# Performance work log

Hardware: AMD Instinct MI355X
Metric: run time of the kernel (lower is better)

The kernel has to match this reference:

```python
import jax, jax.numpy as jnp
import numpy as np

B, T, C, H, N = 2, 1024, 2048, 32, 64
KVH = 8                       # GQA kv heads
KV = KVH * N                  # 512
REP = H // KVH                # 4
EPS = 1e-6
LORA = [96, 96, 64, 256, 64]  # xw, xa, xv, xg, xk lora dims


def rmsnorm(x, w, eps=EPS):
    xf = x.astype(jnp.float32)
    var = jnp.mean(xf * xf, axis=-1, keepdims=True)
    return (w * (xf * jax.lax.rsqrt(var + eps))).astype(x.dtype)


def rotate_half(x):
    x1, x2 = jnp.split(x, 2, axis=-1)
    return jnp.concatenate([-x2, x1], axis=-1)


def rwkv7_scan(r, w, k, v, a, b, state0):
    # r,w,k,v,a,b: [B,T,H,N]; state0: [B,H,N,N] (value x key)
    # per step: S = S*exp(w) + (S@a) b^T + v k^T ; o = S @ r
    def step(S, inp):
        r_t, w_t, k_t, v_t, a_t, b_t = inp  # each [B,H,N]
        sa = jnp.einsum('bhvk,bhk->bhv', S, a_t)
        S = (S * jnp.exp(w_t)[:, :, None, :]
             + sa[..., None] * b_t[:, :, None, :]
             + v_t[..., None] * k_t[:, :, None, :])
        o = jnp.einsum('bhvk,bhk->bhv', S, r_t)
        return S, o
    seqs = tuple(jnp.moveaxis(t, 1, 0) for t in (r, w, k, v, a, b))
    S, o = jax.lax.scan(step, state0, seqs)
    return jnp.moveaxis(o, 0, 1), S


def setup_inputs() -> dict:
    key = jax.random.key(0)
    ks = jax.random.split(key, 24)
    g = lambda i, shape, s=0.02: jax.random.normal(ks[i], shape, jnp.float32) * s
    # real rope cache, theta = 1e6, rotary_dim = N
    pos = jnp.arange(T, dtype=jnp.float32)
    inv = 1.0 / (1e6 ** (jnp.arange(0, N, 2, dtype=jnp.float32) / N))
    ang = pos[:, None] * inv[None, :]
    ang = jnp.concatenate([ang, ang], axis=-1)  # [T, N]
    cos = jnp.broadcast_to(jnp.cos(ang)[None], (B, T, N))
    sin = jnp.broadcast_to(jnp.sin(ang)[None], (B, T, N))
    return dict(
        x_in=jax.random.normal(ks[0], (B, T, C), jnp.float32),
        v_first=jax.random.normal(ks[1], (B, T, KVH, N), jnp.float32),
        k_first=jax.random.normal(ks[2], (B, T, KVH, N), jnp.float32),
        state=jnp.zeros((B, H, N, N), jnp.float32),
        calc_cos=cos, calc_sin=sin,
        ln1=jnp.ones((C,), jnp.float32), ln2=jnp.ones((C,), jnp.float32),
        ln_r=jnp.ones((N,), jnp.float32), ln_k=jnp.ones((N,), jnp.float32),
        wavgk1=g(3, (C, sum(LORA))),
        w0=g(4, (H * N,)), w2=g(5, (LORA[0], H * N)),
        a0=g(6, (H * N,)), a2=g(7, (LORA[1], H * N)),
        v0=g(8, (KV,)), v2=g(9, (LORA[2], KV)),
        k0=g(10, (KV,)), k2=g(11, (LORA[4], KV)),
        g2=g(12, (LORA[3], H * N)),
        r_k=g(13, (H, N)),
        RKV_W=g(14, (C, H * N + 2 * KV)),
        O_W=g(15, (H * N, C)),
        R_bias=g(16, (H * N,)), K_bias=g(17, (KV,)), V_bias=g(18, (KV,)),
    )


def _forward(x_in, v_first, k_first, state, calc_cos, calc_sin,
             ln1, ln2, ln_r, ln_k, wavgk1, w0, w2, a0, a2, v0, v2,
             k0, k2, g2, r_k, RKV_W, O_W, R_bias, K_bias, V_bias):
    x = rmsnorm(x_in, ln1)
    xw, xa, xv, xg, xk = jnp.split(x @ wavgk1, np.cumsum(LORA)[:-1].tolist(), axis=-1)
    r, k, v = jnp.split(x @ RKV_W, [H * N, H * N + KV], axis=-1)
    r = (r + R_bias).reshape(B, T, H, N)
    k = (k + K_bias).reshape(B, T, KVH, N)
    v = (v + V_bias).reshape(B, T, KVH, N)
    r = rmsnorm(r, ln_r)
    k = rmsnorm(k, ln_k)
    cos = calc_cos[:, :, None, :]
    sin = calc_sin[:, :, None, :]
    r = r * cos + rotate_half(r) * sin
    k = k * cos + rotate_half(k) * sin
    # layer_id != 0: sigmoid-gated interpolation toward first-layer v/k
    v = v + (v_first - v) * jax.nn.sigmoid(xv @ v2 + v0).reshape(B, T, KVH, N)
    k = k + (k_first - k) * jax.nn.sigmoid(xk @ k2 + k0).reshape(B, T, KVH, N)
    # GQA repeat (contiguous per kv head, as repeat_kv does)
    k = jnp.repeat(k, REP, axis=2).reshape(B, T, H * N)
    v = jnp.repeat(v, REP, axis=2).reshape(B, T, H * N)
    a = jax.nn.sigmoid(xa @ a2 + a0)
    kh = k.reshape(B, T, H, N)
    kk = (kh / (jnp.linalg.norm(kh, axis=-1, keepdims=True) + 1e-12)).reshape(B, T, H * N)
    w = jnp.tanh(xw) @ w2 + w0
    w = -jax.nn.softplus(-w) - 0.5
    k = k * (1.0 - w + a)
    aa = -kk
    bb = kk * a
    wlog = -jnp.exp(w)
    sh = (B, T, H, N)
    o, state = rwkv7_scan(r, wlog.reshape(sh), k.reshape(sh), v.reshape(sh),
                          aa.reshape(sh), bb.reshape(sh), state)
    xx = o.reshape(B, T, H * N) * (float(N) ** -0.5)
    bonus = ((r * k.reshape(sh) * r_k).sum(axis=-1, keepdims=True)
             * v.reshape(sh)).reshape(B, T, H * N)
    xx = xx + bonus
    out = (xx * (jax.nn.sigmoid(xg) @ g2)) @ O_W
    x_res = x_in + out
    output = rmsnorm(x_res, ln2)
    return output, x[:, -1], state, v_first, k_first, x_res


def reference(x_in, v_first, k_first, state, calc_cos, calc_sin,
              ln1, ln2, ln_r, ln_k, wavgk1, w0, w2, a0, a2, v0, v2,
              k0, k2, g2, r_k, RKV_W, O_W, R_bias, K_bias, V_bias):
    return _forward(x_in, v_first, k_first, state, calc_cos, calc_sin,
                    ln1, ln2, ln_r, ln_k, wavgk1, w0, w2, a0, a2, v0, v2,
                    k0, k2, g2, r_k, RKV_W, O_W, R_bias, K_bias, V_bias)
```

## Files before the change

kernel.cpp:

```cpp
#include <hip/hip_runtime.h>
#include <hip/hip_bf16.h>

#define BT 2
#define TT 1024
#define CC 2048
#define HH 32
#define MM (BT*TT)
#define TCH 512
#define NCH (TT/TCH)
#define RECB 896

typedef __attribute__((ext_vector_type(8))) short short8;
typedef __attribute__((ext_vector_type(4))) float floatx4;

static __device__ __forceinline__ float bf2f(__hip_bfloat16 x){ return __bfloat162float(x); }
static __device__ __forceinline__ __hip_bfloat16 f2bf(float x){ return __float2bfloat16(x); }
static __device__ __forceinline__ float sigm(float x){ return 1.0f/(1.0f + expf(-x)); }
static __device__ __forceinline__ float u2f(unsigned short u){
  union { unsigned int i; float f; } x; x.i = ((unsigned int)u) << 16; return x.f;
}
static __device__ __forceinline__ float ulo(unsigned int u){ return __uint_as_float(u << 16); }
static __device__ __forceinline__ float uhi(unsigned int u){ return __uint_as_float(u & 0xffff0000u); }
static __device__ __forceinline__ unsigned short bfbits(float x){
  __hip_bfloat16 h = f2bf(x);
  unsigned short s; __builtin_memcpy(&s, &h, 2); return s;
}
static __device__ __forceinline__ unsigned int pkbf(float lo, float hi){
  return (unsigned int)bfbits(lo) | ((unsigned int)bfbits(hi) << 16);
}

#if defined(__has_builtin)
#if __has_builtin(__builtin_amdgcn_global_load_lds)
#define HAVE_GLL 1
#endif
#endif

#ifdef HAVE_GLL
static __device__ __forceinline__ void gll16(const void* g, void* l){
  __builtin_amdgcn_global_load_lds(
      (__attribute__((address_space(1))) void*)const_cast<void*>(g),
      (__attribute__((address_space(3))) void*)l,
      16, 0, 0);
}
#endif

#define DPP_ADD(x, ctrl) ((x) + __int_as_float(__builtin_amdgcn_update_dpp(0, __float_as_int(x), (ctrl), 0xF, 0xF, true)))

#if defined(__has_builtin)
#if __has_builtin(__builtin_amdgcn_permlane16_swap) && __has_builtin(__builtin_amdgcn_permlane32_swap)
#define HAVE_PLSWAP 1
#endif
#endif

#ifdef HAVE_PLSWAP
typedef unsigned int uint2v __attribute__((ext_vector_type(2)));
static __device__ __forceinline__ float row16_pair_add(float x){
  unsigned int u = __float_as_uint(x);
  uint2v r = __builtin_amdgcn_permlane16_swap(u, u, false, false);
  return __uint_as_float(r[0]) + __uint_as_float(r[1]);
}
static __device__ __forceinline__ float half32_pair_add(float x){
  unsigned int u = __float_as_uint(x);
  uint2v r = __builtin_amdgcn_permlane32_swap(u, u, false, false);
  return __uint_as_float(r[0]) + __uint_as_float(r[1]);
}
#else
static __device__ __forceinline__ float row16_pair_add(float x){ return x + __shfl_xor(x, 16); }
static __device__ __forceinline__ float half32_pair_add(float x){ return x + __shfl_xor(x, 32); }
#endif

static __device__ __forceinline__ float red8(float x){
  x = DPP_ADD(x, 0xB1);
  x = DPP_ADD(x, 0x4E);
  x = DPP_ADD(x, 0x141);
  return x;
}
static __device__ __forceinline__ float red32(float x){
  x = DPP_ADD(x, 0xB1);
  x = DPP_ADD(x, 0x4E);
  x = DPP_ADD(x, 0x124);
  x = DPP_ADD(x, 0x128);
  return row16_pair_add(x);
}
static __device__ __forceinline__ float red64(float x){
  x = DPP_ADD(x, 0xB1);
  x = DPP_ADD(x, 0x4E);
  x = DPP_ADD(x, 0x124);
  x = DPP_ADD(x, 0x128);
  x = row16_pair_add(x);
  return half32_pair_add(x);
}

__global__ __launch_bounds__(256) void tcvt_kernel(
    const float* __restrict__ W, __hip_bfloat16* __restrict__ Wt,
    int K, int N, int Npad)
{
  __shared__ float tile[32][33];
  const int bn = blockIdx.x*32, bk = blockIdx.y*32;
  const int tx = threadIdx.x & 31, ty0 = threadIdx.x >> 5;
#pragma unroll
  for (int i=0;i<4;++i){
    const int kk = bk + ty0 + i*8;
    float val = 0.f;
    if (kk < K && bn + tx < N) val = W[(size_t)kk*N + bn + tx];
    tile[ty0 + i*8][tx] = val;
  }
  __syncthreads();
#pragma unroll
  for (int i=0;i<4;++i){
    const int nn = bn + ty0 + i*8;
    const int kk = bk + tx;
    if (nn < Npad && kk < K) Wt[(size_t)nn*K + kk] = f2bf(tile[tx][ty0 + i*8]);
  }
}

__global__ __launch_bounds__(256) void rmsnorm1_kernel(
    const float* __restrict__ x_in,
    const float* __restrict__ ln1,
    __hip_bfloat16* __restrict__ x_bf,
    float* __restrict__ x_last)
{
  const int m = blockIdx.x;
  const int tid = threadIdx.x;
  const int c = tid * 8;
  const float* xp = x_in + (size_t)m*CC + c;
  float v[8]; float ss = 0.f;
#pragma unroll
  for (int i=0;i<8;++i){ v[i] = xp[i]; ss += v[i]*v[i]; }
  ss = red64(ss);
  __shared__ float wsum[4];
  if ((tid&63)==0) wsum[tid>>6] = ss;
  __syncthreads();
  ss = wsum[0]+wsum[1]+wsum[2]+wsum[3];
  const float sc = rsqrtf(ss * (1.0f/CC) + 1e-6f);
#pragma unroll
  for (int i=0;i<8;++i) {
    const float y = ln1[c+i] * v[i] * sc;
    x_bf[(size_t)m*CC + c + i] = f2bf(y);
    if ((m % TT) == TT-1) x_last[(size_t)(m/TT)*CC + c + i] = y;
  }
}

template<bool F32OUT, int ACT>
__global__ __launch_bounds__(256) void mgemm(
    const __hip_bfloat16* __restrict__ A, int lda,
    const __hip_bfloat16* __restrict__ Bt,
    void* __restrict__ C, int N, int K)
{
  __shared__ __align__(16) short As[128*32];
  __shared__ __align__(16) short Bs[128*32];
  const int tid = threadIdx.x;
  const int bm = blockIdx.x * 128;
  const int bn = blockIdx.y * 128;
  const int wid = tid >> 6;
  const int lane = tid & 63;
  const int m16 = lane & 15, quad = lane >> 4;
  const int wm = wid & 1, wn = wid >> 1;
  const int lrow = tid >> 2;
  const int lcol = (tid & 3) * 8;

  floatx4 acc[4][4];
#pragma unroll
  for (int i=0;i<4;++i)
#pragma unroll
    for (int j=0;j<4;++j) acc[i][j] = (floatx4){0.f,0.f,0.f,0.f};

  char* asl = (char*)As + tid*16;
  char* bsl = (char*)Bs + tid*16;

  for (int k0 = 0; k0 < K; k0 += 32) {
    __syncthreads();
#ifdef HAVE_GLL
    gll16(A  + (size_t)(bm + lrow)      * lda + k0 + lcol, asl);
    gll16(A  + (size_t)(bm + 64 + lrow) * lda + k0 + lcol, asl + 4096);
    gll16(Bt + (size_t)(bn + lrow)      * K   + k0 + lcol, bsl);
    gll16(Bt + (size_t)(bn + 64 + lrow) * K   + k0 + lcol, bsl + 4096);
#else
    uint4 a0v = *(const uint4*)(const void*)(A  + (size_t)(bm + lrow)      * lda + k0 + lcol);
    uint4 a1v = *(const uint4*)(const void*)(A  + (size_t)(bm + 64 + lrow) * lda + k0 + lcol);
    uint4 b0v = *(const uint4*)(const void*)(Bt + (size_t)(bn + lrow)      * K   + k0 + lcol);
    uint4 b1v = *(const uint4*)(const void*)(Bt + (size_t)(bn + 64 + lrow) * K   + k0 + lcol);
    *(uint4*)(void*)(asl)        = a0v;
    *(uint4*)(void*)(asl + 4096) = a1v;
    *(uint4*)(void*)(bsl)        = b0v;
    *(uint4*)(void*)(bsl + 4096) = b1v;
#endif
    __syncthreads();

    short8 af[4], bfg[4];
#pragma unroll
    for (int mi=0; mi<4; ++mi)
      af[mi] = *(const short8*)(const void*)(As + (wm*64 + mi*16 + m16)*32 + quad*8);
#pragma unroll
    for (int ni=0; ni<4; ++ni)
      bfg[ni] = *(const short8*)(const void*)(Bs + (wn*64 + ni*16 + m16)*32 + quad*8);
#pragma unroll
    for (int mi=0; mi<4; ++mi)
#pragma unroll
      for (int ni=0; ni<4; ++ni)
        acc[mi][ni] = __builtin_amdgcn_mfma_f32_16x16x32_bf16(af[mi], bfg[ni], acc[mi][ni], 0,0,0);
  }

#pragma unroll
  for (int mi=0; mi<4; ++mi) {
    const int row = bm + wm*64 + mi*16 + quad*4;
#pragma unroll
    for (int ni=0; ni<4; ++ni) {
      const int col = bn + wn*64 + ni*16 + m16;
      if (col < N) {
        if (F32OUT) {
          float* cp = (float*)C;
#pragma unroll
          for (int r=0;r<4;++r) cp[(size_t)(row+r)*N + col] = acc[mi][ni][r];
        } else {
          __hip_bfloat16* cp = (__hip_bfloat16*)C;
#pragma unroll
          for (int r=0;r<4;++r) {
            float x = acc[mi][ni][r];
            if (ACT == 1) {
              if (col < 96) x = tanhf(x);
              else if (col >= 256 && col < 512) x = sigm(x);
            }
            cp[(size_t)(row+r)*N + col] = f2bf(x);
          }
        }
      }
    }
  }
}

__global__ __launch_bounds__(256) void prep_kernel(
    const __hip_bfloat16* __restrict__ RKV,
    const __hip_bfloat16* __restrict__ Wpre,
    const __hip_bfloat16* __restrict__ Apre,
    const __hip_bfloat16* __restrict__ Vsig,
    const __hip_bfloat16* __restrict__ Ksig,
    const float* __restrict__ v_first,
    const float* __restrict__ k_first,
    const float* __restrict__ cosp,
    const float* __restrict__ sinp,
    const float* __restrict__ ln_r,
    const float* __restrict__ ln_k,
    const float* __restrict__ r_k,
    const float* __restrict__ w0,
    const float* __restrict__ a0,
    const float* __restrict__ v0,
    const float* __restrict__ k0b,
    const float* __restrict__ R_bias,
    const float* __restrict__ K_bias,
    const float* __restrict__ V_bias,
    char* __restrict__ rec,
    float* __restrict__ bonus,
    int t0)
{
  const int b    = blockIdx.x / TCH;
  const int tloc = blockIdx.x % TCH;
  const int t    = t0 + tloc;
  const int m    = b*TT + t;
  const int tid = threadIdx.x;
  const int h  = tid >> 3;
  const int j  = tid & 7;
  const int hk = h >> 2;
  const int nb = j * 8;
  const int hn = h*64 + nb;
  const int kn = hk*64 + nb;

  const size_t rbase = (size_t)m*3072 + h*64 + nb;
  const size_t kbase = (size_t)m*3072 + 2048 + kn;
  const size_t vbase = kbase + 512;

  float r[8], k[8], v[8];
  float ssr = 0.f, ssk = 0.f;
#pragma unroll
  for (int i=0;i<8;++i) {
    r[i] = bf2f(RKV[rbase+i]) + R_bias[hn+i];
    k[i] = bf2f(RKV[kbase+i]) + K_bias[kn+i];
    v[i] = bf2f(RKV[vbase+i]) + V_bias[kn+i];
    ssr += r[i]*r[i];
    ssk += k[i]*k[i];
  }
  ssr = red8(ssr);
  ssk = red8(ssk);
  const float scr = rsqrtf(ssr*(1.0f/64.0f) + 1e-6f);
  const float sck = rsqrtf(ssk*(1.0f/64.0f) + 1e-6f);
#pragma unroll
  for (int i=0;i<8;++i) {
    r[i] = ln_r[nb+i] * r[i] * scr;
    k[i] = ln_k[nb+i] * k[i] * sck;
  }
  const float sgn = (j < 4) ? -1.0f : 1.0f;
  float rr[8], kr[8];
#pragma unroll
  for (int i=0;i<8;++i) {
    const float cs = cosp[(size_t)m*64 + nb + i];
    const float sn = sinp[(size_t)m*64 + nb + i];
    const float pr = __shfl_xor(r[i], 4);
    const float pk = __shfl_xor(k[i], 4);
    rr[i] = r[i]*cs + sgn*pr*sn;
    kr[i] = k[i]*cs + sgn*pk*sn;
  }
  float av[8], ew[8], wv2[8];
  float ssn = 0.f;
#pragma unroll
  for (int i=0;i<8;++i) {
    const float vs = sigm(bf2f(Vsig[(size_t)m*512 + kn + i]) + v0[kn+i]);
    v[i]  = v[i]  + (v_first[(size_t)m*512 + kn + i] - v[i])  * vs;
    const float ks = sigm(bf2f(Ksig[(size_t)m*512 + kn + i]) + k0b[kn+i]);
    kr[i] = kr[i] + (k_first[(size_t)m*512 + kn + i] - kr[i]) * ks;
    ssn += kr[i]*kr[i];
    av[i] = sigm(bf2f(Apre[(size_t)m*2048 + hn + i]) + a0[hn+i]);
    float wraw = bf2f(Wpre[(size_t)m*2048 + hn + i]) + w0[hn+i];
    const float xs = -wraw;
    const float sp = fmaxf(xs, 0.f) + log1pf(expf(-fabsf(xs)));
    const float wv = -sp - 0.5f;
    wv2[i] = wv;
    ew[i] = expf(-expf(wv));
  }
  ssn = red8(ssn);
  const float inrm = 1.0f / (sqrtf(ssn) + 1e-12f);
  float kf[8], kkv[8];
  float bsum = 0.f;
#pragma unroll
  for (int i=0;i<8;++i) {
    kkv[i] = kr[i] * inrm;
    kf[i]  = kr[i] * (1.0f - wv2[i] + av[i]);
    bsum  += rr[i] * kf[i] * r_k[hn+i];
  }
  bsum = red8(bsum);

  char* base = rec + ((size_t)(b*HH + h)*TCH + tloc)*RECB;
  const int klb = nb >> 1;
#pragma unroll
  for (int p=0;p<4;++p) {
    const int i0 = 2*p, i1 = i0 + 1;
    uint4 Aw;
    Aw.x = __float_as_uint(ew[i0]);
    Aw.y = __float_as_uint(ew[i1]);
    Aw.z = pkbf(rr[i0], rr[i1]);
    Aw.w = pkbf(kf[i0], kf[i1]);
    *(uint4*)(void*)(base + (size_t)(klb + p)*16) = Aw;
    uint2 Bw;
    Bw.x = pkbf(kkv[i0], kkv[i1]);
    Bw.y = pkbf(-kkv[i0]*av[i0], -kkv[i1]*av[i1]);
    *(uint2*)(void*)(base + 512 + (size_t)(klb + p)*8) = Bw;
  }
  short8 vs8;
#pragma unroll
  for (int i=0;i<8;++i) vs8[i] = (short)bfbits(v[i]);
  *(short8*)(void*)(base + 768 + (size_t)nb*2) = vs8;
#pragma unroll
  for (int i=0;i<8;++i)
    bonus[(size_t)m*2048 + hn + i] = bsum * v[i];
}

__global__ __launch_bounds__(256) void scan_kernel(
    const char* __restrict__ rec,
    float* __restrict__ state,
    float* __restrict__ o_out,
    int t0)
{
  const int blk = blockIdx.x;
  const int bh  = blk & 63;
  const int q   = blk >> 6;
  const int b   = bh >> 5, h = bh & 31;
  const int tid = threadIdx.x;
  const int tr  = tid >> 5;
  const int vl0 = q*16 + tr*2;
  const int kl  = tid & 31;
  const int k2  = kl*2;

  const char* base = rec + (size_t)bh * TCH * RECB;
  float* sp0 = state + ((size_t)bh*64 + vl0)*64 + k2;
  float* sp1 = sp0 + 64;
  float S0=sp0[0], S1=sp0[1];
  float S2=sp1[0], S3=sp1[1];

  const char* pA = base + kl*16;
  const char* pB = base + 512 + kl*8;
  const char* pv = base + 768 + vl0*2;

  uint4 Ab[4]; uint2 Bb[4]; unsigned int vb[4];
#pragma unroll
  for (int s=0;s<4;++s){
    Ab[s] = *(const uint4*)(const void*)(pA + s*RECB);
    Bb[s] = *(const uint2*)(const void*)(pB + s*RECB);
    vb[s] = *(const unsigned int*)(const void*)(pv + s*RECB);
  }
  pA += 4*RECB; pB += 4*RECB; pv += 4*RECB;

  int oidx = (b*TT + t0)*CC + h*64 + vl0 - CC;
  float opa = 0.f, opb = 0.f;

#define SCAN_STEP(jj, PF, ST)                                                  \
  {                                                                            \
    const uint4 A  = Ab[jj];                                                   \
    const uint2 Bv = Bb[jj];                                                   \
    const unsigned int vv = vb[jj];                                            \
    if (PF) {                                                                  \
      Ab[jj] = *(const uint4*)(const void*)(pA + jj*RECB);                     \
      Bb[jj] = *(const uint2*)(const void*)(pB + jj*RECB);                     \
      vb[jj] = *(const unsigned int*)(const void*)(pv + jj*RECB);              \
    }                                                                          \
    const float oa = red32(opa);                                               \
    const float ob = red32(opb);                                               \
    const float kk0 = ulo(Bv.x), kk1 = uhi(Bv.x);                              \
    const float saA = red32(S0*kk0 + S1*kk1);                                  \
    const float saB = red32(S2*kk0 + S3*kk1);                                  \
    if (ST && kl == 0) { float2 o2; o2.x = oa; o2.y = ob;                      \
      *(float2*)(void*)(o_out + oidx) = o2; }                                  \
    const float ew0 = __uint_as_float(A.x), ew1 = __uint_as_float(A.y);        \
    const float bb0 = ulo(Bv.y), bb1 = uhi(Bv.y);                              \
    const float kf0 = ulo(A.w),  kf1 = uhi(A.w);                               \
    const float r0  = ulo(A.z),  r1  = uhi(A.z);                               \
    const float vfa = ulo(vv),   vfb = uhi(vv);                                \
    S0 = S0*ew0 + saA*bb0 + vfa*kf0;                                           \
    S1 = S1*ew1 + saA*bb1 + vfa*kf1;                                           \
    S2 = S2*ew0 + saB*bb0 + vfb*kf0;                                           \
    S3 = S3*ew1 + saB*bb1 + vfb*kf1;                                           \
    opa = S0*r0 + S1*r1;                                                       \
    opb = S2*r0 + S3*r1;                                                       \
    oidx += CC;                                                                \
  }

  SCAN_STEP(0, true, 0)
  SCAN_STEP(1, true, 1)
  SCAN_STEP(2, true, 1)
  SCAN_STEP(3, true, 1)
  pA += 4*RECB; pB += 4*RECB; pv += 4*RECB;

  for (int t = 4; t < TCH-4; t += 4) {
    SCAN_STEP(0, true, 1)
    SCAN_STEP(1, true, 1)
    SCAN_STEP(2, true, 1)
    SCAN_STEP(3, true, 1)
    pA += 4*RECB; pB += 4*RECB; pv += 4*RECB;
  }
  SCAN_STEP(0, false, 1)
  SCAN_STEP(1, false, 1)
  SCAN_STEP(2, false, 1)
  SCAN_STEP(3, false, 1)
#undef SCAN_STEP

  {
    const float oa = red32(opa);
    const float ob = red32(opb);
    if (kl == 0) { float2 o2; o2.x = oa; o2.y = ob;
      *(float2*)(void*)(o_out + oidx) = o2; }
  }

  sp0[0]=S0; sp0[1]=S1;
  sp1[0]=S2; sp1[1]=S3;
}

__global__ void xxg_kernel(const float* __restrict__ o_in,
                           const float* __restrict__ bonus,
                           const __hip_bfloat16* __restrict__ G,
                           __hip_bfloat16* __restrict__ xxg)
{
  int i = blockIdx.x*256 + threadIdx.x;
  xxg[i] = f2bf((o_in[i]*0.125f + bonus[i]) * bf2f(G[i]));
}

__global__ __launch_bounds__(256) void final_kernel(
    const float* __restrict__ x_in,
    const float* __restrict__ OUTb,
    const float* __restrict__ ln2,
    float* __restrict__ seg0,
    float* __restrict__ seg5)
{
  const int m = blockIdx.x;
  const int tid = threadIdx.x;
  const int c = tid*8;
  const float* xp = x_in + (size_t)m*CC + c;
  const float* op = OUTb + (size_t)m*CC + c;
  float xr[8]; float ss = 0.f;
#pragma unroll
  for (int i=0;i<8;++i){ xr[i] = xp[i] + op[i]; ss += xr[i]*xr[i]; }
#pragma unroll
  for (int i=0;i<8;++i) seg5[(size_t)m*CC + c + i] = xr[i];
  ss = red64(ss);
  __shared__ float wsum[4];
  if ((tid&63)==0) wsum[tid>>6] = ss;
  __syncthreads();
  ss = wsum[0]+wsum[1]+wsum[2]+wsum[3];
  const float sc = rsqrtf(ss*(1.0f/CC) + 1e-6f);
#pragma unroll
  for (int i=0;i<8;++i) seg0[(size_t)m*CC + c + i] = ln2[c+i] * xr[i] * sc;
}

extern "C" void kernel_launch(void* const* d_in, const int* in_sizes, int n_in,
                              void* d_out, int out_size, void* d_ws, size_t ws_size,
                              hipStream_t stream)
{
  (void)in_sizes; (void)n_in; (void)out_size; (void)ws_size;
  const float* x_in   = (const float*)d_in[0];
  const float* v_first= (const float*)d_in[1];
  const float* k_first= (const float*)d_in[2];
  const float* state0 = (const float*)d_in[3];
  const float* cosp   = (const float*)d_in[4];
  const float* sinp   = (const float*)d_in[5];
  const float* ln1    = (const float*)d_in[6];
  const float* ln2    = (const float*)d_in[7];
  const float* ln_r   = (const float*)d_in[8];
  const float* ln_k   = (const float*)d_in[9];
  const float* wavgk1 = (const float*)d_in[10];
  const float* w0     = (const float*)d_in[11];
  const float* w2     = (const float*)d_in[12];
  const float* a0     = (const float*)d_in[13];
  const float* a2     = (const float*)d_in[14];
  const float* v0     = (const float*)d_in[15];
  const float* v2     = (const float*)d_in[16];
  const float* k0b    = (const float*)d_in[17];
  const float* k2     = (const float*)d_in[18];
  const float* g2     = (const float*)d_in[19];
  const float* r_k    = (const float*)d_in[20];
  const float* RKV_W  = (const float*)d_in[21];
  const float* O_W    = (const float*)d_in[22];
  const float* R_bias = (const float*)d_in[23];
  const float* K_bias = (const float*)d_in[24];
  const float* V_bias = (const float*)d_in[25];

  float* out  = (float*)d_out;
  float* seg0 = out;
  float* seg1 = out + 4194304;
  float* seg2 = out + 4198400;
  float* seg3 = out + 4460544;
  float* seg4 = out + 5509120;
  float* seg5 = out + 6557696;

  char* ws = (char*)d_ws;
  const size_t OFF_STF   = 0;
  const size_t OFF_OWT   = 1048576;
  const size_t OFF_G     = 9437184;
  const size_t OFF_VSIG  = 17825792;
  const size_t OFF_KSIG  = 19922944;
  const size_t OFF_WPRE  = 22020096;
  const size_t OFF_APRE  = 30408704;
  const size_t OFF_RKV   = 38797312;
  const size_t OFF_XBF   = 51380224;
  const size_t OFF_Y1    = 59768832;
  const size_t OFF_WT    = 62128128;
  const size_t OFF_WAVT  = OFF_WT;
  const size_t OFF_RKVT  = OFF_WAVT + 2621440;
  const size_t OFF_W2T   = OFF_RKVT + 12582912;
  const size_t OFF_A2T   = OFF_W2T  + 393216;
  const size_t OFF_V2T   = OFF_A2T  + 393216;
  const size_t OFF_K2T   = OFF_V2T  + 65536;
  const size_t OFF_G2T   = OFF_K2T  + 65536;
  const size_t OFF_REC   = OFF_WT;
  const size_t OFF_XXG   = OFF_XBF;
  const size_t OFF_OUT   = OFF_WPRE;

  float*          stf   = (float*)(ws + OFF_STF);
  __hip_bfloat16* owt   = (__hip_bfloat16*)(ws + OFF_OWT);
  __hip_bfloat16* Gbuf  = (__hip_bfloat16*)(ws + OFF_G);
  __hip_bfloat16* Vsig  = (__hip_bfloat16*)(ws + OFF_VSIG);
  __hip_bfloat16* Ksig  = (__hip_bfloat16*)(ws + OFF_KSIG);
  __hip_bfloat16* Wpre  = (__hip_bfloat16*)(ws + OFF_WPRE);
  __hip_bfloat16* Apre  = (__hip_bfloat16*)(ws + OFF_APRE);
  __hip_bfloat16* RKV   = (__hip_bfloat16*)(ws + OFF_RKV);
  __hip_bfloat16* x_bf  = (__hip_bfloat16*)(ws + OFF_XBF);
  __hip_bfloat16* Y1    = (__hip_bfloat16*)(ws + OFF_Y1);
  __hip_bfloat16* wavt  = (__hip_bfloat16*)(ws + OFF_WAVT);
  __hip_bfloat16* rkvt  = (__hip_bfloat16*)(ws + OFF_RKVT);
  __hip_bfloat16* w2t   = (__hip_bfloat16*)(ws + OFF_W2T);
  __hip_bfloat16* a2t   = (__hip_bfloat16*)(ws + OFF_A2T);
  __hip_bfloat16* v2t   = (__hip_bfloat16*)(ws + OFF_V2T);
  __hip_bfloat16* k2t   = (__hip_bfloat16*)(ws + OFF_K2T);
  __hip_bfloat16* g2t   = (__hip_bfloat16*)(ws + OFF_G2T);
  char*           rec   = ws + OFF_REC;
  __hip_bfloat16* xxg   = (__hip_bfloat16*)(ws + OFF_XXG);
  float*          OUTb  = (float*)(ws + OFF_OUT);

  float* o_st = seg0;
  float* b_st = seg5;

  tcvt_kernel<<<dim3(20, 64), 256, 0, stream>>>(wavgk1, wavt, 2048, 576, 640);
  tcvt_kernel<<<dim3(96, 64), 256, 0, stream>>>(RKV_W,  rkvt, 2048, 3072, 3072);
  tcvt_kernel<<<dim3(64, 64), 256, 0, stream>>>(O_W,    owt,  2048, 2048, 2048);
  tcvt_kernel<<<dim3(64,  3), 256, 0, stream>>>(w2,     w2t,    96, 2048, 2048);
  tcvt_kernel<<<dim3(64,  3), 256, 0, stream>>>(a2,     a2t,    96, 2048, 2048);
  tcvt_kernel<<<dim3(16,  2), 256, 0, stream>>>(v2,     v2t,    64,  512,  512);
  tcvt_kernel<<<dim3(16,  2), 256, 0, stream>>>(k2,     k2t,    64,  512,  512);
  tcvt_kernel<<<dim3(64,  8), 256, 0, stream>>>(g2,     g2t,   256, 2048, 2048);

  rmsnorm1_kernel<<<MM, 256, 0, stream>>>(x_in, ln1, x_bf, seg1);
  mgemm<false,1><<<dim3(16,  5), 256, 0, stream>>>(x_bf, CC, wavt, Y1,   576, 2048);
  mgemm<false,0><<<dim3(16, 24), 256, 0, stream>>>(x_bf, CC, rkvt, RKV, 3072, 2048);
  mgemm<false,0><<<dim3(16, 16), 256, 0, stream>>>(Y1+0,   576, w2t, Wpre, 2048, 96);
  mgemm<false,0><<<dim3(16, 16), 256, 0, stream>>>(Y1+96,  576, a2t, Apre, 2048, 96);
  mgemm<false,0><<<dim3(16,  4), 256, 0, stream>>>(Y1+192, 576, v2t, Vsig,  512, 64);
  mgemm<false,0><<<dim3(16,  4), 256, 0, stream>>>(Y1+512, 576, k2t, Ksig,  512, 64);
  mgemm<false,0><<<dim3(16, 16), 256, 0, stream>>>(Y1+256, 576, g2t, Gbuf, 2048, 256);

  hipMemcpyAsync(stf, state0, (size_t)1048576, hipMemcpyDeviceToDevice, stream);
  for (int c = 0; c < NCH; ++c) {
    const int t0 = c*TCH;
    prep_kernel<<<BT*TCH, 256, 0, stream>>>(RKV, Wpre, Apre, Vsig, Ksig, v_first, k_first,
                                            cosp, sinp, ln_r, ln_k, r_k, w0, a0, v0, k0b,
                                            R_bias, K_bias, V_bias, rec, b_st, t0);
    scan_kernel<<<BT*HH*4, 256, 0, stream>>>(rec, stf, o_st, t0);
  }
  hipMemcpyAsync(seg2, stf, (size_t)1048576, hipMemcpyDeviceToDevice, stream);

  xxg_kernel<<<(MM*CC)/256, 256, 0, stream>>>(o_st, b_st, Gbuf, xxg);
  mgemm<true,0><<<dim3(16, 16), 256, 0, stream>>>(xxg, CC, owt, OUTb, 2048, 2048);
  final_kernel<<<MM, 256, 0, stream>>>(x_in, OUTb, ln2, seg0, seg5);

  hipMemcpyAsync(seg3, v_first, (size_t)1048576*4, hipMemcpyDeviceToDevice, stream);
  hipMemcpyAsync(seg4, k_first, (size_t)1048576*4, hipMemcpyDeviceToDevice, stream);
}
```

Measured before the change: 665.0 us.

## Fuse two recurrence steps per iteration to shorten serial reduction chain

The scan now processes timesteps in pairs. The second step's S·a projection is expanded algebraically in terms of the pre-update state: S·(ew1∘a2), the S·a1 term scaled by b1·a2, and v1 times k1·a2. This makes all cross-lane reductions for both steps independent of each other, cutting the serial dependency from two reduction rounds per pair to one. In exchange it does more red32 reductions per step and changes floating-point rounding order.

```diff
diff --git a/kernel.cpp b/kernel.cpp
--- a/kernel.cpp
+++ b/kernel.cpp
@@ -379,73 +379,110 @@
   const char* pB = base + 512 + kl*8;
   const char* pv = base + 768 + vl0*2;
 
-  uint4 Ab[4]; uint2 Bb[4]; unsigned int vb[4];
-#pragma unroll
-  for (int s=0;s<4;++s){
-    Ab[s] = *(const uint4*)(const void*)(pA + s*RECB);
-    Bb[s] = *(const uint2*)(const void*)(pB + s*RECB);
-    vb[s] = *(const unsigned int*)(const void*)(pv + s*RECB);
-  }
+  uint4 A1x, A2x, A1y, A2y;
+  uint2 B1x, B2x, B1y, B2y;
+  unsigned int v1x, v2x, v1y, v2y;
+
+  A1x = *(const uint4*)(const void*)(pA);
+  B1x = *(const uint2*)(const void*)(pB);
+  v1x = *(const unsigned int*)(const void*)(pv);
+  A2x = *(const uint4*)(const void*)(pA + RECB);
+  B2x = *(const uint2*)(const void*)(pB + RECB);
+  v2x = *(const unsigned int*)(const void*)(pv + RECB);
+  A1y = *(const uint4*)(const void*)(pA + 2*RECB);
+  B1y = *(const uint2*)(const void*)(pB + 2*RECB);
+  v1y = *(const unsigned int*)(const void*)(pv + 2*RECB);
+  A2y = *(const uint4*)(const void*)(pA + 3*RECB);
+  B2y = *(const uint2*)(const void*)(pB + 3*RECB);
+  v2y = *(const unsigned int*)(const void*)(pv + 3*RECB);
   pA += 4*RECB; pB += 4*RECB; pv += 4*RECB;
 
-  int oidx = (b*TT + t0)*CC + h*64 + vl0 - CC;
-  float opa = 0.f, opb = 0.f;
-
-#define SCAN_STEP(jj, PF, ST)                                                  \
+  int oidx = (b*TT + t0)*CC + h*64 + vl0 - 2*CC;
+  float p1a = 0.f, p1b = 0.f, p2a = 0.f, p2b = 0.f;
+
+#define PAIR(A1,B1,v1,A2,B2,v2, PF, PFOFF, ST)                                 \
   {                                                                            \
-    const uint4 A  = Ab[jj];                                                   \
-    const uint2 Bv = Bb[jj];                                                   \
-    const unsigned int vv = vb[jj];                                            \
+            \
+    const float o1a = red32(p1a);                                              \
+    const float o1b = red32(p1b);                                              \
+    const float o2a = red32(p2a);                                              \
+    const float o2b = red32(p2b);                                              \
+    if (ST && kl == 0) {                                                       \
+      float2 oA; oA.x = o1a; oA.y = o1b;                                       \
+      float2 oB; oB.x = o2a; oB.y = o2b;                                       \
+      *(float2*)(void*)(o_out + oidx) = oA;                                    \
+      *(float2*)(void*)(o_out + oidx + CC) = oB;                               \
+    }                                                                          \
+    oidx += 2*CC;                                                              \
+                                       \
+    const float kk20 = ulo(B2.x), kk21 = uhi(B2.x);                            \
+    const float bb10 = ulo(B1.y), bb11 = uhi(B1.y);                            \
+    const float kf10 = ulo(A1.w), kf11 = uhi(A1.w);                            \
+    const float c1 = red32(bb10*kk20 + bb11*kk21);                             \
+    const float c2 = red32(kf10*kk20 + kf11*kk21);                             \
+                             \
+    const float kk10 = ulo(B1.x), kk11 = uhi(B1.x);                            \
+    const float ew10 = __uint_as_float(A1.x), ew11 = __uint_as_float(A1.y);    \
+    const float e0 = ew10*kk20, e1 = ew11*kk21;                                \
+    const float d1A = red32(S0*kk10 + S1*kk11);                                \
+    const float d1B = red32(S2*kk10 + S3*kk11);                                \
+    const float d2A = red32(S0*e0 + S1*e1);                                    \
+    const float d2B = red32(S2*e0 + S3*e1);                                    \
+    const float vf1a = ulo(v1), vf1b = uhi(v1);                                \
+    const float vf2a = ulo(v2), vf2b = uhi(v2);                                \
+                                                \
+    S0 = S0*ew10 + d1A*bb10 + vf1a*kf10;                                       \
+    S1 = S1*ew11 + d1A*bb11 + vf1a*kf11;                                       \
+    S2 = S2*ew10 + d1B*bb10 + vf1b*kf10;                                       \
+    S3 = S3*ew11 + d1B*bb11 + vf1b*kf11;                                       \
+    p1a = S0*ulo(A1.z) + S1*uhi(A1.z);                                         \
+    p1b = S2*ulo(A1.z) + S3*uhi(A1.z);                                         \
+                                                           \
+    const float sa2A = d2A + d1A*c1 + vf1a*c2;                                 \
+    const float sa2B = d2B + d1B*c1 + vf1b*c2;                                 \
+    const float ew20 = __uint_as_float(A2.x), ew21 = __uint_as_float(A2.y);    \
+    const float bb20 = ulo(B2.y), bb21 = uhi(B2.y);                            \
+    const float kf20 = ulo(A2.w), kf21 = uhi(A2.w);                            \
+    S0 = S0*ew20 + sa2A*bb20 + vf2a*kf20;                                      \
+    S1 = S1*ew21 + sa2A*bb21 + vf2a*kf21;                                      \
+    S2 = S2*ew20 + sa2B*bb20 + vf2b*kf20;                                      \
+    S3 = S3*ew21 + sa2B*bb21 + vf2b*kf21;                                      \
+    p2a = S0*ulo(A2.z) + S1*uhi(A2.z);                                         \
+    p2b = S2*ulo(A2.z) + S3*uhi(A2.z);                                         \
     if (PF) {                                                                  \
-      Ab[jj] = *(const uint4*)(const void*)(pA + jj*RECB);                     \
-      Bb[jj] = *(const uint2*)(const void*)(pB + jj*RECB);                     \
-      vb[jj] = *(const unsigned int*)(const void*)(pv + jj*RECB);              \
+      A1 = *(const uint4*)(const void*)(pA + (PFOFF));                         \
+      B1 = *(const uint2*)(const void*)(pB + (PFOFF));                         \
+      v1 = *(const unsigned int*)(const void*)(pv + (PFOFF));                  \
+      A2 = *(const uint4*)(const void*)(pA + (PFOFF) + RECB);                  \
+      B2 = *(const uint2*)(const void*)(pB + (PFOFF) + RECB);                  \
+      v2 = *(const unsigned int*)(const void*)(pv + (PFOFF) + RECB);           \
     }                                                                          \
-    const float oa = red32(opa);                                               \
-    const float ob = red32(opb);                                               \
-    const float kk0 = ulo(Bv.x), kk1 = uhi(Bv.x);                              \
-    const float saA = red32(S0*kk0 + S1*kk1);                                  \
-    const float saB = red32(S2*kk0 + S3*kk1);                                  \
-    if (ST && kl == 0) { float2 o2; o2.x = oa; o2.y = ob;                      \
-      *(float2*)(void*)(o_out + oidx) = o2; }                                  \
-    const float ew0 = __uint_as_float(A.x), ew1 = __uint_as_float(A.y);        \
-    const float bb0 = ulo(Bv.y), bb1 = uhi(Bv.y);                              \
-    const float kf0 = ulo(A.w),  kf1 = uhi(A.w);                               \
-    const float r0  = ulo(A.z),  r1  = uhi(A.z);                               \
-    const float vfa = ulo(vv),   vfb = uhi(vv);                                \
-    S0 = S0*ew0 + saA*bb0 + vfa*kf0;                                           \
-    S1 = S1*ew1 + saA*bb1 + vfa*kf1;                                           \
-    S2 = S2*ew0 + saB*bb0 + vfb*kf0;                                           \
-    S3 = S3*ew1 + saB*bb1 + vfb*kf1;                                           \
-    opa = S0*r0 + S1*r1;                                                       \
-    opb = S2*r0 + S3*r1;                                                       \
-    oidx += CC;                                                                \
-  }
-
-  SCAN_STEP(0, true, 0)
-  SCAN_STEP(1, true, 1)
-  SCAN_STEP(2, true, 1)
-  SCAN_STEP(3, true, 1)
+  }
+
+  PAIR(A1x,B1x,v1x,A2x,B2x,v2x, 1, 0,        0)
+  PAIR(A1y,B1y,v1y,A2y,B2y,v2y, 1, 2*RECB,   1)
   pA += 4*RECB; pB += 4*RECB; pv += 4*RECB;
 
-  for (int t = 4; t < TCH-4; t += 4) {
-    SCAN_STEP(0, true, 1)
-    SCAN_STEP(1, true, 1)
-    SCAN_STEP(2, true, 1)
-    SCAN_STEP(3, true, 1)
+  for (int p = 2; p < TCH/2 - 2; p += 2) {
+    PAIR(A1x,B1x,v1x,A2x,B2x,v2x, 1, 0,      1)
+    PAIR(A1y,B1y,v1y,A2y,B2y,v2y, 1, 2*RECB, 1)
     pA += 4*RECB; pB += 4*RECB; pv += 4*RECB;
   }
-  SCAN_STEP(0, false, 1)
-  SCAN_STEP(1, false, 1)
-  SCAN_STEP(2, false, 1)
-  SCAN_STEP(3, false, 1)
-#undef SCAN_STEP
+  PAIR(A1x,B1x,v1x,A2x,B2x,v2x, 0, 0, 1)
+  PAIR(A1y,B1y,v1y,A2y,B2y,v2y, 0, 0, 1)
+#undef PAIR
 
   {
-    const float oa = red32(opa);
-    const float ob = red32(opb);
-    if (kl == 0) { float2 o2; o2.x = oa; o2.y = ob;
-      *(float2*)(void*)(o_out + oidx) = o2; }
+    const float o1a = red32(p1a);
+    const float o1b = red32(p1b);
+    const float o2a = red32(p2a);
+    const float o2b = red32(p2b);
+    if (kl == 0) {
+      float2 oA; oA.x = o1a; oA.y = o1b;
+      float2 oB; oB.x = o2a; oB.y = o2b;
+      *(float2*)(void*)(o_out + oidx) = oA;
+      *(float2*)(void*)(o_out + oidx + CC) = oB;
+    }
   }
 
   sp0[0]=S0; sp0[1]=S1;
```

Result: no change. 673.5 us (+1.3%).

## Stage scan record groups through double-buffered LDS with cooperative loads

Applied to the files above, without the earlier changes.

The scan kernel previously had every thread prefetch its own slices of each 896-byte time-step record from global memory into registers, four steps ahead. It now loads groups of four records (3584 bytes) cooperatively, with 224 threads each copying 16 bytes into one of two shared-memory buffers. The next group is staged while the current one is consumed. This aims to cut redundant, uncoalesced global loads on the serial scan path. In exchange it adds a block-wide barrier every four steps and LDS reads on the critical path. The synchronous copy path is used unless HAVE_GLL is defined.

```diff
diff --git a/kernel.cpp b/kernel.cpp
--- a/kernel.cpp
+++ b/kernel.cpp
@@ -9,6 +9,7 @@
 #define TCH 512
 #define NCH (TT/TCH)
 #define RECB 896
+#define GRPB 3584
 
 typedef __attribute__((ext_vector_type(8))) short short8;
 typedef __attribute__((ext_vector_type(4))) float floatx4;
@@ -359,6 +360,9 @@
     float* __restrict__ o_out,
     int t0)
 {
+  __shared__ __align__(16) char lds0[GRPB];
+  __shared__ __align__(16) char lds1[GRPB];
+
   const int blk = blockIdx.x;
   const int bh  = blk & 63;
   const int q   = blk >> 6;
@@ -375,32 +379,28 @@
   float S0=sp0[0], S1=sp0[1];
   float S2=sp1[0], S3=sp1[1];
 
-  const char* pA = base + kl*16;
-  const char* pB = base + 512 + kl*8;
-  const char* pv = base + 768 + vl0*2;
-
-  uint4 Ab[4]; uint2 Bb[4]; unsigned int vb[4];
-#pragma unroll
-  for (int s=0;s<4;++s){
-    Ab[s] = *(const uint4*)(const void*)(pA + s*RECB);
-    Bb[s] = *(const uint2*)(const void*)(pB + s*RECB);
-    vb[s] = *(const unsigned int*)(const void*)(pv + s*RECB);
-  }
-  pA += 4*RECB; pB += 4*RECB; pv += 4*RECB;
+#ifdef HAVE_GLL
+#define STAGE(g, DST)                                                          \
+  do { if (tid < 224)                                                          \
+    gll16(base + (size_t)(g)*GRPB + tid*16, (DST) + tid*16);                   \
+  } while (0)
+#else
+#define STAGE(g, DST)                                                          \
+  do { if (tid < 224)                                                          \
+    *(uint4*)(void*)((DST) + tid*16) =                                         \
+      *(const uint4*)(const void*)(base + (size_t)(g)*GRPB + tid*16);          \
+  } while (0)
+#endif
 
   int oidx = (b*TT + t0)*CC + h*64 + vl0 - CC;
   float opa = 0.f, opb = 0.f;
 
-#define SCAN_STEP(jj, PF, ST)                                                  \
+#define STEP(L, jj, ST)                                                        \
   {                                                                            \
-    const uint4 A  = Ab[jj];                                                   \
-    const uint2 Bv = Bb[jj];                                                   \
-    const unsigned int vv = vb[jj];                                            \
-    if (PF) {                                                                  \
-      Ab[jj] = *(const uint4*)(const void*)(pA + jj*RECB);                     \
-      Bb[jj] = *(const uint2*)(const void*)(pB + jj*RECB);                     \
-      vb[jj] = *(const unsigned int*)(const void*)(pv + jj*RECB);              \
-    }                                                                          \
+    const uint4 A  = *(const uint4*)(const void*)((L) + (jj)*RECB + kl*16);    \
+    const uint2 Bv = *(const uint2*)(const void*)((L) + (jj)*RECB + 512 + kl*8);\
+    const unsigned int vv =                                                    \
+      *(const unsigned int*)(const void*)((L) + (jj)*RECB + 768 + vl0*2);      \
     const float oa = red32(opa);                                               \
     const float ob = red32(opb);                                               \
     const float kk0 = ulo(Bv.x), kk1 = uhi(Bv.x);                              \
@@ -422,24 +422,33 @@
     oidx += CC;                                                                \
   }
 
-  SCAN_STEP(0, true, 0)
-  SCAN_STEP(1, true, 1)
-  SCAN_STEP(2, true, 1)
-  SCAN_STEP(3, true, 1)
-  pA += 4*RECB; pB += 4*RECB; pv += 4*RECB;
-
-  for (int t = 4; t < TCH-4; t += 4) {
-    SCAN_STEP(0, true, 1)
-    SCAN_STEP(1, true, 1)
-    SCAN_STEP(2, true, 1)
-    SCAN_STEP(3, true, 1)
-    pA += 4*RECB; pB += 4*RECB; pv += 4*RECB;
-  }
-  SCAN_STEP(0, false, 1)
-  SCAN_STEP(1, false, 1)
-  SCAN_STEP(2, false, 1)
-  SCAN_STEP(3, false, 1)
-#undef SCAN_STEP
+#define GROUP(L, S0FLAG) STEP(L,0,S0FLAG) STEP(L,1,1) STEP(L,2,1) STEP(L,3,1)
+
+  STAGE(0, lds0);
+  __syncthreads();
+  STAGE(1, lds1);
+
+  GROUP(lds0, 0)
+  __syncthreads();
+  STAGE(2, lds0);
+  GROUP(lds1, 1)
+  __syncthreads();
+  STAGE(3, lds1);
+
+  for (int g = 2; g < TCH/4 - 2; g += 2) {
+    GROUP(lds0, 1)
+    __syncthreads();
+    STAGE(g+2, lds0);
+    GROUP(lds1, 1)
+    __syncthreads();
+    STAGE(g+3, lds1);
+  }
+  GROUP(lds0, 1)
+  __syncthreads();
+  GROUP(lds1, 1)
+#undef GROUP
+#undef STEP
+#undef STAGE
 
   {
     const float oa = red32(opa);
```

After: 683.8 us. 2.8% more time.
